# Kernel tuning notes

Measured on AMD Instinct MI355X. Metric: run time of the kernel, lower is better.

The kernel has to match this reference:

```python
import itertools
import jax, jax.numpy as jnp
import numpy as np

GRID = 16384      # self.shape = (GRID,)
LAYERS = 8        # num_layers
SPAN = 2          # span = (2,)
K = 2 * SPAN + 1  # kernel size = 5 (ninputs)
NPOS = 2 ** K     # 32 possible boolean input combos
BATCH = 32
M = 4096          # x width; GRID % M == 0
STRIDE = GRID // M

# bitmask: all 2^K boolean input combinations, shape (NPOS, K)
_BITMASK = jnp.asarray(list(itertools.product(range(2), repeat=K)), dtype=jnp.float32)


def setup_inputs() -> dict:
    key = jax.random.key(0)
    k1, k2 = jax.random.split(key)
    x = jax.random.uniform(k1, (BATCH, M), dtype=jnp.float32)
    toggle_gates = jax.random.uniform(k2, (LAYERS, NPOS, GRID), dtype=jnp.float32)
    return {"x": x, "toggle_gates": toggle_gates}


def _convolve(state):
    # torch convolve(): offsets 0..K-1 via wrap-around roll, then spatial roll by
    # -SPAN to center the window -> neighbor n+i-SPAN (mod GRID) at kernel idx i.
    # jnp.roll(state, SPAN - i) gives out[:, n] = state[:, n + i - SPAN mod GRID].
    return jnp.stack([jnp.roll(state, SPAN - i, axis=1) for i in range(K)], axis=-1)  # (B, N, K)


def reference(x, toggle_gates):
    tw = jax.nn.sigmoid(toggle_gates)  # (L, NPOS, N)
    # embed(): scatter x evenly into the grid, rest is scratch (zeros)
    state = jnp.zeros((x.shape[0], GRID), dtype=x.dtype).at[:, ::STRIDE].set(x)

    def step(s, tw_layer):
        conv = _convolve(s)  # (B, N, K)
        # weight[c, b, n] = prod_i (1 - |bitmask[c, i] - conv[b, n, i]|)
        w = jnp.prod(1.0 - jnp.abs(_BITMASK[:, None, None, :] - conv[None]), axis=-1)  # (C, B, N)
        new = jnp.clip(jnp.einsum('cbn,cn->bn', w, tw_layer), 0.0, 1.0)
        return new, None

    state, _ = jax.lax.scan(step, state, tw)
    # forward returns state[slices] = state[:, ::STRIDE]
    return state[:, ::STRIDE]
```

## Files before the change

### kernel.cpp

```cpp
#include <hip/hip_runtime.h>

#define GRID_N 16384
#define NLAYERS 8
#define NPOS 32
#define BATCH 32
#define MW 4096
#define TILE 32
#define HALO 16
#define WBUF 64
#define ROWP 36

struct F2 { float a, b; };

__global__ __launch_bounds__(512, 4) void ASIC_44186623541335_kernel(
    const float* __restrict__ x,
    const float* __restrict__ tg,
    float* __restrict__ out)
{
    __shared__ __align__(16) float st[2][WBUF][ROWP];
    __shared__ __align__(16) float twl[2][WBUF][ROWP];

    const int tid = threadIdx.x;
    const int tx  = tid & 63;
    const int ty  = tid >> 6;
    const int c0  = 4 * ty;
    const int start = blockIdx.x * TILE;
    const int gcol  = (start - HALO + tx) & (GRID_N - 1);

    float pf[4];
    #pragma unroll
    for (int k = 0; k < 4; ++k)
        pf[k] = tg[(size_t)(c0 + k) * GRID_N + gcol];

    for (int f = tid; f < WBUF * BATCH; f += 512) {
        const int j = f >> 5;
        const int b = f & 31;
        const int g = (start - HALO + j) & (GRID_N - 1);
        st[0][j][b] = ((g & 3) == 0) ? x[b * MW + (g >> 2)] : 0.0f;
    }

    {
        float4 sg;
        sg.x = __builtin_amdgcn_rcpf(1.0f + __expf(-pf[0]));
        sg.y = __builtin_amdgcn_rcpf(1.0f + __expf(-pf[1]));
        sg.z = __builtin_amdgcn_rcpf(1.0f + __expf(-pf[2]));
        sg.w = __builtin_amdgcn_rcpf(1.0f + __expf(-pf[3]));
        *(float4*)&twl[0][tx][c0] = sg;
        #pragma unroll
        for (int k = 0; k < 4; ++k)
            pf[k] = tg[(size_t)NPOS * GRID_N + (size_t)(c0 + k) * GRID_N + gcol];
    }
    __syncthreads();

    #pragma unroll
    for (int l = 0; l < NLAYERS; ++l) {
        const int h     = 2 * (NLAYERS - 1 - l);
        const int ncols = TILE + 2 * h;
        const int j     = (HALO - h) + tx;
        const int rb    = l & 1, wb = rb ^ 1;

        if (l < NLAYERS - 1) {
            float4 sg;
            sg.x = __builtin_amdgcn_rcpf(1.0f + __expf(-pf[0]));
            sg.y = __builtin_amdgcn_rcpf(1.0f + __expf(-pf[1]));
            sg.z = __builtin_amdgcn_rcpf(1.0f + __expf(-pf[2]));
            sg.w = __builtin_amdgcn_rcpf(1.0f + __expf(-pf[3]));
            *(float4*)&twl[wb][tx][c0] = sg;
        }
        if (l + 2 < NLAYERS) {
            const float* tn = tg + (size_t)(l + 2) * NPOS * GRID_N;
            #pragma unroll
            for (int k = 0; k < 4; ++k)
                pf[k] = tn[(size_t)(c0 + k) * GRID_N + gcol];
        }

        if (tx < ncols) {
            float tw[32];
            #pragma unroll
            for (int k = 0; k < 8; ++k) {
                const float4 q = *(const float4*)&twl[rb][j][4 * k];
                tw[4 * k]     = q.x; tw[4 * k + 1] = q.y;
                tw[4 * k + 2] = q.z; tw[4 * k + 3] = q.w;
            }
            float d0[16];
            #pragma unroll
            for (int r = 0; r < 16; ++r) d0[r] = tw[16 + r] - tw[r];

            float4 S0 = *(const float4*)&st[rb][j - 2][c0];
            float4 S1 = *(const float4*)&st[rb][j - 1][c0];
            float4 S2 = *(const float4*)&st[rb][j    ][c0];
            float4 S3 = *(const float4*)&st[rb][j + 1][c0];
            float4 S4 = *(const float4*)&st[rb][j + 2][c0];

            float4 res;
            #pragma unroll
            for (int p = 0; p < 2; ++p) {
                const float s0a = p ? S0.z : S0.x, s0b = p ? S0.w : S0.y;
                const float s1a = p ? S1.z : S1.x, s1b = p ? S1.w : S1.y;
                const float s2a = p ? S2.z : S2.x, s2b = p ? S2.w : S2.y;
                const float s3a = p ? S3.z : S3.x, s3b = p ? S3.w : S3.y;
                const float s4a = p ? S4.z : S4.x, s4b = p ? S4.w : S4.y;

                F2 u[16];
                #pragma unroll
                for (int r = 0; r < 16; ++r) {
                    u[r].a = fmaf(s0a, d0[r], tw[r]);
                    u[r].b = fmaf(s0b, d0[r], tw[r]);
                }
                #pragma unroll
                for (int r = 0; r < 8; ++r) {
                    const float da = u[8 + r].a - u[r].a, db = u[8 + r].b - u[r].b;
                    u[r].a = fmaf(s1a, da, u[r].a);
                    u[r].b = fmaf(s1b, db, u[r].b);
                }
                #pragma unroll
                for (int r = 0; r < 4; ++r) {
                    const float da = u[4 + r].a - u[r].a, db = u[4 + r].b - u[r].b;
                    u[r].a = fmaf(s2a, da, u[r].a);
                    u[r].b = fmaf(s2b, db, u[r].b);
                }
                #pragma unroll
                for (int r = 0; r < 2; ++r) {
                    const float da = u[2 + r].a - u[r].a, db = u[2 + r].b - u[r].b;
                    u[r].a = fmaf(s3a, da, u[r].a);
                    u[r].b = fmaf(s3b, db, u[r].b);
                }
                const float da = u[1].a - u[0].a, db = u[1].b - u[0].b;
                float ra = fmaf(s4a, da, u[0].a);
                float rbv = fmaf(s4b, db, u[0].b);
                ra  = fminf(fmaxf(ra, 0.0f), 1.0f);
                rbv = fminf(fmaxf(rbv, 0.0f), 1.0f);
                if (p) { res.z = ra; res.w = rbv; } else { res.x = ra; res.y = rbv; }
            }
            *(float4*)&st[wb][j][c0] = res;
        }
        __syncthreads();
    }

    if (tid < 256) {
        const int c4 = tid & 7;
        const int b  = tid >> 3;
        out[b * MW + (start >> 2) + c4] = st[0][HALO + 4 * c4][b];
    }
}

extern "C" void kernel_launch(void* const* d_in, const int* in_sizes, int n_in,
                              void* d_out, int out_size, void* d_ws, size_t ws_size,
                              hipStream_t stream) {
    const float* x  = (const float*)d_in[0];
    const float* tg = (const float*)d_in[1];
    float* out = (float*)d_out;
    ASIC_44186623541335_kernel<<<GRID_N / TILE, 512, 0, stream>>>(x, tg, out);
}
```

Baseline: 81.24 us.

## Replace per-layer block barriers with wave barriers and batch gate loads per four layers

Each wave only reads and writes its own four batch columns of the state, so the state is updated in place in a single buffer and the per-layer __syncthreads becomes a wave barrier. Gate weights are now prefetched and passed through the sigmoid four layers at a time into a four-slot shared buffer, which needs only two block barriers at the half-way point. The initial scatter loop is re-indexed so consecutive threads touch consecutive grid positions. In exchange it uses more registers (16 prefetched values), more shared memory for gates, and no longer fully unrolls the layer loop.

```diff
diff --git a/kernel.cpp b/kernel.cpp
--- a/kernel.cpp
+++ b/kernel.cpp
@@ -10,15 +10,13 @@
 #define WBUF 64
 #define ROWP 36
 
-struct F2 { float a, b; };
-
 __global__ __launch_bounds__(512, 4) void ASIC_44186623541335_kernel(
     const float* __restrict__ x,
     const float* __restrict__ tg,
     float* __restrict__ out)
 {
-    __shared__ __align__(16) float st[2][WBUF][ROWP];
-    __shared__ __align__(16) float twl[2][WBUF][ROWP];
+    __shared__ __align__(16) float st[WBUF][ROWP];
+    __shared__ __align__(16) float twl[4][WBUF][ROWP];
 
     const int tid = threadIdx.x;
     const int tx  = tid & 63;
@@ -27,120 +25,115 @@
     const int start = blockIdx.x * TILE;
     const int gcol  = (start - HALO + tx) & (GRID_N - 1);
 
-    float pf[4];
+    float pf[16];
     #pragma unroll
-    for (int k = 0; k < 4; ++k)
-        pf[k] = tg[(size_t)(c0 + k) * GRID_N + gcol];
+    for (int l4 = 0; l4 < 4; ++l4)
+        #pragma unroll
+        for (int k = 0; k < 4; ++k)
+            pf[l4 * 4 + k] = tg[((size_t)l4 * NPOS + c0 + k) * GRID_N + gcol];
 
     for (int f = tid; f < WBUF * BATCH; f += 512) {
-        const int j = f >> 5;
-        const int b = f & 31;
+        const int b = f >> 6;
+        const int j = f & 63;
         const int g = (start - HALO + j) & (GRID_N - 1);
-        st[0][j][b] = ((g & 3) == 0) ? x[b * MW + (g >> 2)] : 0.0f;
+        st[j][b] = ((g & 3) == 0) ? x[b * MW + (g >> 2)] : 0.0f;
     }
 
-    {
+    #pragma unroll
+    for (int l4 = 0; l4 < 4; ++l4) {
         float4 sg;
-        sg.x = __builtin_amdgcn_rcpf(1.0f + __expf(-pf[0]));
-        sg.y = __builtin_amdgcn_rcpf(1.0f + __expf(-pf[1]));
-        sg.z = __builtin_amdgcn_rcpf(1.0f + __expf(-pf[2]));
-        sg.w = __builtin_amdgcn_rcpf(1.0f + __expf(-pf[3]));
-        *(float4*)&twl[0][tx][c0] = sg;
+        sg.x = __builtin_amdgcn_rcpf(1.0f + __expf(-pf[l4 * 4 + 0]));
+        sg.y = __builtin_amdgcn_rcpf(1.0f + __expf(-pf[l4 * 4 + 1]));
+        sg.z = __builtin_amdgcn_rcpf(1.0f + __expf(-pf[l4 * 4 + 2]));
+        sg.w = __builtin_amdgcn_rcpf(1.0f + __expf(-pf[l4 * 4 + 3]));
+        *(float4*)&twl[l4][tx][c0] = sg;
+    }
+    #pragma unroll
+    for (int l4 = 0; l4 < 4; ++l4)
         #pragma unroll
         for (int k = 0; k < 4; ++k)
-            pf[k] = tg[(size_t)NPOS * GRID_N + (size_t)(c0 + k) * GRID_N + gcol];
-    }
+            pf[l4 * 4 + k] = tg[((size_t)(4 + l4) * NPOS + c0 + k) * GRID_N + gcol];
     __syncthreads();
 
-    #pragma unroll
     for (int l = 0; l < NLAYERS; ++l) {
         const int h     = 2 * (NLAYERS - 1 - l);
         const int ncols = TILE + 2 * h;
         const int j     = (HALO - h) + tx;
-        const int rb    = l & 1, wb = rb ^ 1;
-
-        if (l < NLAYERS - 1) {
-            float4 sg;
-            sg.x = __builtin_amdgcn_rcpf(1.0f + __expf(-pf[0]));
-            sg.y = __builtin_amdgcn_rcpf(1.0f + __expf(-pf[1]));
-            sg.z = __builtin_amdgcn_rcpf(1.0f + __expf(-pf[2]));
-            sg.w = __builtin_amdgcn_rcpf(1.0f + __expf(-pf[3]));
-            *(float4*)&twl[wb][tx][c0] = sg;
-        }
-        if (l + 2 < NLAYERS) {
-            const float* tn = tg + (size_t)(l + 2) * NPOS * GRID_N;
-            #pragma unroll
-            for (int k = 0; k < 4; ++k)
-                pf[k] = tn[(size_t)(c0 + k) * GRID_N + gcol];
-        }
 
         if (tx < ncols) {
             float tw[32];
             #pragma unroll
             for (int k = 0; k < 8; ++k) {
-                const float4 q = *(const float4*)&twl[rb][j][4 * k];
+                const float4 q = *(const float4*)&twl[l & 3][j][4 * k];
                 tw[4 * k]     = q.x; tw[4 * k + 1] = q.y;
                 tw[4 * k + 2] = q.z; tw[4 * k + 3] = q.w;
             }
-            float d0[16];
-            #pragma unroll
-            for (int r = 0; r < 16; ++r) d0[r] = tw[16 + r] - tw[r];
-
-            float4 S0 = *(const float4*)&st[rb][j - 2][c0];
-            float4 S1 = *(const float4*)&st[rb][j - 1][c0];
-            float4 S2 = *(const float4*)&st[rb][j    ][c0];
-            float4 S3 = *(const float4*)&st[rb][j + 1][c0];
-            float4 S4 = *(const float4*)&st[rb][j + 2][c0];
 
             float4 res;
             #pragma unroll
             for (int p = 0; p < 2; ++p) {
-                const float s0a = p ? S0.z : S0.x, s0b = p ? S0.w : S0.y;
-                const float s1a = p ? S1.z : S1.x, s1b = p ? S1.w : S1.y;
-                const float s2a = p ? S2.z : S2.x, s2b = p ? S2.w : S2.y;
-                const float s3a = p ? S3.z : S3.x, s3b = p ? S3.w : S3.y;
-                const float s4a = p ? S4.z : S4.x, s4b = p ? S4.w : S4.y;
+                const float2 S0 = *(const float2*)&st[j - 2][c0 + 2 * p];
+                const float2 S1 = *(const float2*)&st[j - 1][c0 + 2 * p];
+                const float2 S2 = *(const float2*)&st[j    ][c0 + 2 * p];
+                const float2 S3 = *(const float2*)&st[j + 1][c0 + 2 * p];
+                const float2 S4 = *(const float2*)&st[j + 2][c0 + 2 * p];
 
-                F2 u[16];
+                float ua[16], ub[16];
                 #pragma unroll
                 for (int r = 0; r < 16; ++r) {
-                    u[r].a = fmaf(s0a, d0[r], tw[r]);
-                    u[r].b = fmaf(s0b, d0[r], tw[r]);
+                    const float d = tw[16 + r] - tw[r];
+                    ua[r] = fmaf(S0.x, d, tw[r]);
+                    ub[r] = fmaf(S0.y, d, tw[r]);
                 }
                 #pragma unroll
                 for (int r = 0; r < 8; ++r) {
-                    const float da = u[8 + r].a - u[r].a, db = u[8 + r].b - u[r].b;
-                    u[r].a = fmaf(s1a, da, u[r].a);
-                    u[r].b = fmaf(s1b, db, u[r].b);
+                    const float da = ua[8 + r] - ua[r], db = ub[8 + r] - ub[r];
+                    ua[r] = fmaf(S1.x, da, ua[r]);
+                    ub[r] = fmaf(S1.y, db, ub[r]);
                 }
                 #pragma unroll
                 for (int r = 0; r < 4; ++r) {
-                    const float da = u[4 + r].a - u[r].a, db = u[4 + r].b - u[r].b;
-                    u[r].a = fmaf(s2a, da, u[r].a);
-                    u[r].b = fmaf(s2b, db, u[r].b);
+                    const float da = ua[4 + r] - ua[r], db = ub[4 + r] - ub[r];
+                    ua[r] = fmaf(S2.x, da, ua[r]);
+                    ub[r] = fmaf(S2.y, db, ub[r]);
                 }
                 #pragma unroll
                 for (int r = 0; r < 2; ++r) {
-                    const float da = u[2 + r].a - u[r].a, db = u[2 + r].b - u[r].b;
-                    u[r].a = fmaf(s3a, da, u[r].a);
-                    u[r].b = fmaf(s3b, db, u[r].b);
+                    const float da = ua[2 + r] - ua[r], db = ub[2 + r] - ub[r];
+                    ua[r] = fmaf(S3.x, da, ua[r]);
+                    ub[r] = fmaf(S3.y, db, ub[r]);
                 }
-                const float da = u[1].a - u[0].a, db = u[1].b - u[0].b;
-                float ra = fmaf(s4a, da, u[0].a);
-                float rbv = fmaf(s4b, db, u[0].b);
-                ra  = fminf(fmaxf(ra, 0.0f), 1.0f);
-                rbv = fminf(fmaxf(rbv, 0.0f), 1.0f);
-                if (p) { res.z = ra; res.w = rbv; } else { res.x = ra; res.y = rbv; }
+                const float da = ua[1] - ua[0], db = ub[1] - ub[0];
+                float ra = fmaf(S4.x, da, ua[0]);
+                float rb = fmaf(S4.y, db, ub[0]);
+                ra = fminf(fmaxf(ra, 0.0f), 1.0f);
+                rb = fminf(fmaxf(rb, 0.0f), 1.0f);
+                if (p) { res.z = ra; res.w = rb; } else { res.x = ra; res.y = rb; }
             }
-            *(float4*)&st[wb][j][c0] = res;
+            *(float4*)&st[j][c0] = res;
         }
-        __syncthreads();
+        __builtin_amdgcn_wave_barrier();
+
+        if (l == 3) {
+            __syncthreads();
+            #pragma unroll
+            for (int l4 = 0; l4 < 4; ++l4) {
+                float4 sg;
+                sg.x = __builtin_amdgcn_rcpf(1.0f + __expf(-pf[l4 * 4 + 0]));
+                sg.y = __builtin_amdgcn_rcpf(1.0f + __expf(-pf[l4 * 4 + 1]));
+                sg.z = __builtin_amdgcn_rcpf(1.0f + __expf(-pf[l4 * 4 + 2]));
+                sg.w = __builtin_amdgcn_rcpf(1.0f + __expf(-pf[l4 * 4 + 3]));
+                *(float4*)&twl[l4][tx][c0] = sg;
+            }
+            __syncthreads();
+        }
     }
 
+    __syncthreads();
     if (tid < 256) {
         const int c4 = tid & 7;
         const int b  = tid >> 3;
-        out[b * MW + (start >> 2) + c4] = st[0][HALO + 4 * c4][b];
+        out[b * MW + (start >> 2) + c4] = st[HALO + 4 * c4][b];
     }
 }
 
```

Result: no change. 82.11 us (+1.1%).
